# Kernel optimization log

Hardware: AMD Instinct MI355X
Metric: run time of the kernel (lower is better)

The kernel has to match this reference:

```python
import jax, jax.numpy as jnp
import numpy as np

B, S, E = 2, 2048, 2048
H, KVH = 16, 4
HD = E // H          # 128
REP = H // KVH       # 4
THETA = 100000.0


def _rope_cos_sin(seqlen, head_dim, theta=THETA):
    # Faithful to precompute_pos_cis: exponent is arange(0, d, 2) (NOT divided by d)
    freqs = 1.0 / theta ** jnp.arange(0, head_dim, 2, dtype=jnp.float32)[: head_dim // 2]
    ang = jnp.outer(jnp.arange(seqlen, dtype=jnp.float32), freqs)  # (S, HD/2)
    return jnp.cos(ang), jnp.sin(ang)


def _apply_rotary(t, cos, sin):
    # t: (B, S, h, HD) -> complex pairs along last dim
    b, s, h, d = t.shape
    t = t.astype(jnp.float32).reshape(b, s, h, d // 2, 2)
    tr, ti = t[..., 0], t[..., 1]
    c = cos[None, :, None, :]
    sn = sin[None, :, None, :]
    out_r = tr * c - ti * sn
    out_i = tr * sn + ti * c
    return jnp.stack([out_r, out_i], axis=-1).reshape(b, s, h, d)


def setup_inputs() -> dict:
    key = jax.random.key(0)
    ks = jax.random.split(key, 9)
    sc_e = 1.0 / np.sqrt(E)
    return {
        "x": jax.random.normal(ks[0], (B, S, E), jnp.float32),
        "wq": jax.random.normal(ks[1], (E, H * HD), jnp.float32) * sc_e,
        "bq": jax.random.normal(ks[2], (H * HD,), jnp.float32) * 0.01,
        "wk": jax.random.normal(ks[3], (E, KVH * HD), jnp.float32) * sc_e,
        "bk": jax.random.normal(ks[4], (KVH * HD,), jnp.float32) * 0.01,
        "wv": jax.random.normal(ks[5], (E, KVH * HD), jnp.float32) * sc_e,
        "bv": jax.random.normal(ks[6], (KVH * HD,), jnp.float32) * 0.01,
        "wo": jax.random.normal(ks[7], (H * HD, E), jnp.float32) * sc_e,
        "bo": jax.random.normal(ks[8], (E,), jnp.float32) * 0.01,
    }


def reference(x, wq, bq, wk, bk, wv, bv, wo, bo):
    b, s, _ = x.shape
    xq = (x @ wq + bq).reshape(b, s, H, HD)
    xk = (x @ wk + bk).reshape(b, s, KVH, HD)
    xv = (x @ wv + bv).reshape(b, s, KVH, HD)

    cos, sin = _rope_cos_sin(s, HD)
    xq = _apply_rotary(xq, cos, sin)
    xk = _apply_rotary(xk, cos, sin)

    # GQA: group query heads over shared KV heads instead of materializing repeat_kv
    q = xq.transpose(0, 2, 1, 3).reshape(b, KVH, REP, s, HD)  # (B, G, R, S, D)
    k = xk.transpose(0, 2, 1, 3)                               # (B, G, S, D)
    v = xv.astype(jnp.float32).transpose(0, 2, 1, 3)           # (B, G, S, D)

    scores = jnp.einsum("bgrqd,bgkd->bgrqk", q, k) / jnp.sqrt(jnp.float32(HD))
    causal = jnp.tril(jnp.ones((s, s), dtype=bool))
    scores = jnp.where(causal[None, None, None], scores, jnp.float32(-jnp.inf))
    attn = jax.nn.softmax(scores, axis=-1)
    out = jnp.einsum("bgrqk,bgkd->bgrqd", attn, v)  # (B, G, R, S, D)
    out = out.reshape(b, H, s, HD).transpose(0, 2, 1, 3).reshape(b, s, H * HD)
    return out @ wo + bo
```

## Files before the change

### kernel.cpp

```cpp
#include <hip/hip_runtime.h>
#include <math.h>

#define BB 2
#define SS 2048
#define EE 2048
#define HH 16
#define KVH 4
#define HD 128

typedef __attribute__((ext_vector_type(8))) short short8;
typedef __attribute__((ext_vector_type(4))) float f32x4;

__device__ __forceinline__ short f2b(float f) {
  unsigned u = __float_as_uint(f);
  unsigned r = (u + 0x7fffu + ((u >> 16) & 1u)) >> 16;
  return (short)r;
}

__device__ __forceinline__ void async_load16(const void* g, void* l) {
  __builtin_amdgcn_global_load_lds(
      (const __attribute__((address_space(1))) void*)g,
      (__attribute__((address_space(3))) void*)l, 16, 0, 0);
}

__device__ __forceinline__ float rope_freq(int jp) {
  return exp2f(-(float)(2 * jp) * 16.609640474436812f);
}

__global__ void f32_to_bf16(const float* __restrict__ in, short* __restrict__ out) {
  int i = (blockIdx.x * 256 + threadIdx.x) * 8;
  float4 a = *(const float4*)(in + i);
  float4 b = *(const float4*)(in + i + 4);
  short8 c;
  c[0] = f2b(a.x); c[1] = f2b(a.y); c[2] = f2b(a.z); c[3] = f2b(a.w);
  c[4] = f2b(b.x); c[5] = f2b(b.y); c[6] = f2b(b.z); c[7] = f2b(b.w);
  *(short8*)(out + i) = c;
}

__global__ void transpose_f2b(const float* __restrict__ in, short* __restrict__ out,
                              int K, int N) {
  __shared__ short tile[32][33];
  int n0 = blockIdx.x * 32, k0 = blockIdx.y * 32;
  int tx = threadIdx.x, ty = threadIdx.y;
#pragma unroll
  for (int i = 0; i < 32; i += 8)
    tile[ty + i][tx] = f2b(in[(size_t)(k0 + ty + i) * N + n0 + tx]);
  __syncthreads();
#pragma unroll
  for (int i = 0; i < 32; i += 8)
    out[(size_t)(n0 + ty + i) * K + k0 + tx] = tile[tx][ty + i];
}

__global__ __launch_bounds__(512, 4) void gemm_qkv(
    const short* __restrict__ A, const short* __restrict__ Bt,
    const float* __restrict__ bq, const float* __restrict__ bk,
    const float* __restrict__ bv,
    short* __restrict__ qbuf, short* __restrict__ kbuf, short* __restrict__ vtr) {
  __shared__ __align__(16) short Sm[256 * 136];
  short* Bl = Sm + 16384;
  const int K = EE;
  int t = threadIdx.x, lane = t & 63, w = t >> 6;
  int lj = lane & 15, lr = lane >> 4;
  int wm = (w >> 1) * 64, wn = (w & 1) * 64;
  int m0 = blockIdx.x * 256, n0 = blockIdx.y * 128;
  const short* Ab = A + (size_t)m0 * K;
  const short* Bb = Bt + (size_t)n0 * K;
  int srow = t >> 3, scol = (t & 7) * 8;
  char* ldsA = (char*)Sm + w * 1024;
  char* ldsB = (char*)Sm + 32768 + w * 1024;
  f32x4 acc[4][4] = {};
  for (int k0 = 0; k0 < K; k0 += 64) {
#pragma unroll
    for (int q = 0; q < 4; q++)
      async_load16(Ab + (size_t)(q * 64 + srow) * K + k0 + scol, ldsA + q * 8192);
#pragma unroll
    for (int q = 0; q < 2; q++)
      async_load16(Bb + (size_t)(q * 64 + srow) * K + k0 + scol, ldsB + q * 8192);
    __syncthreads();
    short8 a0[4], a1[4], b0[4], b1[4];
#pragma unroll
    for (int i = 0; i < 4; i++) {
      a0[i] = *(const short8*)&Sm[(wm + i * 16 + lj) * 64 + lr * 8];
      a1[i] = *(const short8*)&Sm[(wm + i * 16 + lj) * 64 + 32 + lr * 8];
    }
#pragma unroll
    for (int j = 0; j < 4; j++) {
      b0[j] = *(const short8*)&Bl[(wn + j * 16 + lj) * 64 + lr * 8];
      b1[j] = *(const short8*)&Bl[(wn + j * 16 + lj) * 64 + 32 + lr * 8];
    }
#pragma unroll
    for (int i = 0; i < 4; i++)
#pragma unroll
      for (int j = 0; j < 4; j++) {
        acc[i][j] = __builtin_amdgcn_mfma_f32_16x16x32_bf16(a0[i], b0[j], acc[i][j], 0, 0, 0);
        acc[i][j] = __builtin_amdgcn_mfma_f32_16x16x32_bf16(a1[i], b1[j], acc[i][j], 0, 0, 0);
      }
    __syncthreads();
  }
  if (n0 < 2048) {
#pragma unroll
    for (int j = 0; j < 4; j++) {
      int d = wn + j * 16 + lj;
      float bias = bq[n0 + d];
      float freq = rope_freq(d >> 1);
      bool odd = (d & 1) != 0;
#pragma unroll
      for (int i = 0; i < 4; i++)
#pragma unroll
        for (int r = 0; r < 4; r++) {
          int mloc = wm + i * 16 + lr * 4 + r;
          int s = (m0 + mloc) & (SS - 1);
          float val = acc[i][j][r] + bias;
          float other = __shfl_xor(val, 1, 64);
          float ang = (float)s * freq;
          float cs = cosf(ang), sn = sinf(ang);
          float res = odd ? (other * sn + val * cs) : (val * cs - other * sn);
          Sm[mloc * 136 + d] = f2b(res);
        }
    }
  } else if (n0 < 2560) {
    int base = n0 - 2048;
#pragma unroll
    for (int j = 0; j < 4; j++) {
      int d = wn + j * 16 + lj;
      float bias = bk[base + d];
      float freq = rope_freq(d >> 1);
      bool odd = (d & 1) != 0;
#pragma unroll
      for (int i = 0; i < 4; i++)
#pragma unroll
        for (int r = 0; r < 4; r++) {
          int mloc = wm + i * 16 + lr * 4 + r;
          int s = (m0 + mloc) & (SS - 1);
          float val = acc[i][j][r] + bias;
          float other = __shfl_xor(val, 1, 64);
          float ang = (float)s * freq;
          float cs = cosf(ang), sn = sinf(ang);
          float res = odd ? (other * sn + val * cs) : (val * cs - other * sn);
          Sm[mloc * 136 + d] = f2b(res);
        }
    }
  } else {
    int base = n0 - 2560;
#pragma unroll
    for (int j = 0; j < 4; j++) {
      int d = wn + j * 16 + lj;
      float bias = bv[base + d];
#pragma unroll
      for (int i = 0; i < 4; i++)
#pragma unroll
        for (int r = 0; r < 4; r++) {
          int mloc = wm + i * 16 + lr * 4 + r;
          Sm[d * 264 + mloc] = f2b(acc[i][j][r] + bias);
        }
    }
  }
  __syncthreads();
  if (n0 < 2048) {
    int r0 = t >> 4, ch = t & 15;
#pragma unroll
    for (int p = 0; p < 8; p++) {
      int row = p * 32 + r0;
      *(short8*)(qbuf + (size_t)(m0 + row) * 2048 + n0 + ch * 8) =
          *(const short8*)&Sm[row * 136 + ch * 8];
    }
  } else if (n0 < 2560) {
    int r0 = t >> 4, ch = t & 15;
    int kvh = (n0 - 2048) >> 7;
    int b = m0 >> 11, s0 = m0 & (SS - 1);
    short* dst = kbuf + ((size_t)(b * KVH + kvh) * SS + s0) * HD;
#pragma unroll
    for (int p = 0; p < 8; p++) {
      int row = p * 32 + r0;
      *(short8*)(dst + (size_t)row * HD + ch * 8) = *(const short8*)&Sm[row * 136 + ch * 8];
    }
  } else {
    int r0 = t >> 5, ch = t & 31;
    int kvh = (n0 - 2560) >> 7;
    int b = m0 >> 11, s0 = m0 & (SS - 1);
    short* dst = vtr + ((size_t)(b * KVH + kvh) * HD) * SS + s0;
#pragma unroll
    for (int p = 0; p < 8; p++) {
      int dl = p * 16 + r0;
      *(short8*)(dst + (size_t)dl * SS + ch * 8) = *(const short8*)&Sm[dl * 264 + ch * 8];
    }
  }
}

__global__ __launch_bounds__(256) void attn_kernel(
    const short* __restrict__ qb, const short* __restrict__ kb,
    const short* __restrict__ vt, short* __restrict__ ao) {
  __shared__ __align__(16) short Kl[64 * 128];
  __shared__ __align__(16) short Vl[128 * 64];
  __shared__ __align__(16) short Pl[4 * 16 * 64];
  int t = threadIdx.x, lane = t & 63, w = t >> 6;
  int lj = lane & 15, lr = lane >> 4;
  int id = blockIdx.x + (blockIdx.y << 5) + (blockIdx.z << 9);
  int swz = (id & 7) * 128 + (id >> 3);
  int qt = swz & 31, h = (swz >> 5) & 15, b = swz >> 9;
  int kvh = h >> 2;
  int qb0 = qt * 64;
  const short* qbase = qb + (size_t)(b * SS) * 2048 + h * HD;
  const short* kbase = kb + (size_t)(b * KVH + kvh) * SS * HD;
  const short* vbase = vt + (size_t)(b * KVH + kvh) * HD * SS;
  short8 aq[4];
  int sq = qb0 + w * 16 + lj;
#pragma unroll
  for (int kk = 0; kk < 4; kk++)
    aq[kk] = *(const short8*)(qbase + (size_t)sq * 2048 + kk * 32 + lr * 8);
  f32x4 O[8] = {};
  const float NEG = -1e30f;
  float mrow[4] = {NEG, NEG, NEG, NEG};
  float lrow[4] = {0.f, 0.f, 0.f, 0.f};
  const float scale = 0.088388347648318447f;
  int nkt = qt + 1;
  for (int kt = 0; kt < nkt; ++kt) {
    short8 gk[4], gv[4];
#pragma unroll
    for (int i = 0; i < 4; i++) {
      gk[i] = *(const short8*)(kbase + (size_t)(kt * 64 + i * 16 + (t >> 4)) * HD + (t & 15) * 8);
      gv[i] = *(const short8*)(vbase + (size_t)(i * 32 + (t >> 3)) * SS + kt * 64 + (t & 7) * 8);
    }
#pragma unroll
    for (int i = 0; i < 4; i++) {
      *(short8*)&Kl[(i * 16 + (t >> 4)) * 128 + (t & 15) * 8] = gk[i];
      *(short8*)&Vl[(i * 32 + (t >> 3)) * 64 + (t & 7) * 8] = gv[i];
    }
    __syncthreads();
    f32x4 S[4];
#pragma unroll
    for (int nt = 0; nt < 4; nt++) {
      f32x4 sc = {};
#pragma unroll
      for (int kk = 0; kk < 4; kk++) {
        short8 bk_ = *(const short8*)&Kl[(nt * 16 + lj) * 128 + kk * 32 + lr * 8];
        sc = __builtin_amdgcn_mfma_f32_16x16x32_bf16(aq[kk], bk_, sc, 0, 0, 0);
      }
      S[nt] = sc;
    }
    int rowg = qb0 + w * 16 + lr * 4;
#pragma unroll
    for (int nt = 0; nt < 4; nt++) {
      int colg = kt * 64 + nt * 16 + lj;
#pragma unroll
      for (int r = 0; r < 4; r++) {
        float v = S[nt][r] * scale;
        if (colg > rowg + r) v = NEG;
        S[nt][r] = v;
      }
    }
    float alpha[4];
#pragma unroll
    for (int r = 0; r < 4; r++) {
      float m_ = fmaxf(fmaxf(S[0][r], S[1][r]), fmaxf(S[2][r], S[3][r]));
#pragma unroll
      for (int off = 1; off < 16; off <<= 1) m_ = fmaxf(m_, __shfl_xor(m_, off, 64));
      float mn = fmaxf(mrow[r], m_);
      alpha[r] = __expf(mrow[r] - mn);
      mrow[r] = mn;
    }
    float ls[4] = {0.f, 0.f, 0.f, 0.f};
#pragma unroll
    for (int nt = 0; nt < 4; nt++)
#pragma unroll
      for (int r = 0; r < 4; r++) {
        float p = __expf(S[nt][r] - mrow[r]);
        ls[r] += p;
        Pl[(w * 16 + lr * 4 + r) * 64 + nt * 16 + lj] = f2b(p);
      }
#pragma unroll
    for (int r = 0; r < 4; r++) {
      float s_ = ls[r];
#pragma unroll
      for (int off = 1; off < 16; off <<= 1) s_ += __shfl_xor(s_, off, 64);
      lrow[r] = lrow[r] * alpha[r] + s_;
    }
#pragma unroll
    for (int jt = 0; jt < 8; jt++)
#pragma unroll
      for (int r = 0; r < 4; r++) O[jt][r] *= alpha[r];
#pragma unroll
    for (int kk = 0; kk < 2; kk++) {
      short8 ap = *(const short8*)&Pl[(w * 16 + lj) * 64 + kk * 32 + lr * 8];
#pragma unroll
      for (int jt = 0; jt < 8; jt++) {
        short8 bv_ = *(const short8*)&Vl[(jt * 16 + lj) * 64 + kk * 32 + lr * 8];
        O[jt] = __builtin_amdgcn_mfma_f32_16x16x32_bf16(ap, bv_, O[jt], 0, 0, 0);
      }
    }
    __syncthreads();
  }
  size_t obase = (size_t)(b * SS + qb0 + w * 16) * 2048 + h * HD;
#pragma unroll
  for (int jt = 0; jt < 8; jt++)
#pragma unroll
    for (int r = 0; r < 4; r++) {
      int row = lr * 4 + r;
      ao[obase + (size_t)row * 2048 + jt * 16 + lj] = f2b(O[jt][r] / lrow[r]);
    }
}

__global__ __launch_bounds__(512, 4) void gemm_out(
    const short* __restrict__ A, const short* __restrict__ Bt,
    const float* __restrict__ bo, float* __restrict__ out) {
  __shared__ __align__(16) short Sm[24576];
  short* Bl = Sm + 16384;
  const int K = EE;
  int t = threadIdx.x, lane = t & 63, w = t >> 6;
  int lj = lane & 15, lr = lane >> 4;
  int wm = (w >> 1) * 64, wn = (w & 1) * 64;
  int m0 = blockIdx.x * 256, n0 = blockIdx.y * 128;
  const short* Ab = A + (size_t)m0 * K;
  const short* Bb = Bt + (size_t)n0 * K;
  int srow = t >> 3, scol = (t & 7) * 8;
  char* ldsA = (char*)Sm + w * 1024;
  char* ldsB = (char*)Sm + 32768 + w * 1024;
  f32x4 acc[4][4] = {};
  for (int k0 = 0; k0 < K; k0 += 64) {
#pragma unroll
    for (int q = 0; q < 4; q++)
      async_load16(Ab + (size_t)(q * 64 + srow) * K + k0 + scol, ldsA + q * 8192);
#pragma unroll
    for (int q = 0; q < 2; q++)
      async_load16(Bb + (size_t)(q * 64 + srow) * K + k0 + scol, ldsB + q * 8192);
    __syncthreads();
    short8 a0[4], a1[4], b0[4], b1[4];
#pragma unroll
    for (int i = 0; i < 4; i++) {
      a0[i] = *(const short8*)&Sm[(wm + i * 16 + lj) * 64 + lr * 8];
      a1[i] = *(const short8*)&Sm[(wm + i * 16 + lj) * 64 + 32 + lr * 8];
    }
#pragma unroll
    for (int j = 0; j < 4; j++) {
      b0[j] = *(const short8*)&Bl[(wn + j * 16 + lj) * 64 + lr * 8];
      b1[j] = *(const short8*)&Bl[(wn + j * 16 + lj) * 64 + 32 + lr * 8];
    }
#pragma unroll
    for (int i = 0; i < 4; i++)
#pragma unroll
      for (int j = 0; j < 4; j++) {
        acc[i][j] = __builtin_amdgcn_mfma_f32_16x16x32_bf16(a0[i], b0[j], acc[i][j], 0, 0, 0);
        acc[i][j] = __builtin_amdgcn_mfma_f32_16x16x32_bf16(a1[i], b1[j], acc[i][j], 0, 0, 0);
      }
    __syncthreads();
  }
#pragma unroll
  for (int j = 0; j < 4; j++) {
    int n = n0 + wn + j * 16 + lj;
    float bias = bo[n];
#pragma unroll
    for (int i = 0; i < 4; i++)
#pragma unroll
      for (int r = 0; r < 4; r++) {
        int m = m0 + wm + i * 16 + lr * 4 + r;
        out[(size_t)m * 2048 + n] = acc[i][j][r] + bias;
      }
  }
}

extern "C" void kernel_launch(void* const* d_in, const int* in_sizes, int n_in,
                              void* d_out, int out_size, void* d_ws, size_t ws_size,
                              hipStream_t stream) {
  const float* x  = (const float*)d_in[0];
  const float* wq = (const float*)d_in[1];
  const float* bq = (const float*)d_in[2];
  const float* wk = (const float*)d_in[3];
  const float* bk = (const float*)d_in[4];
  const float* wv = (const float*)d_in[5];
  const float* bv = (const float*)d_in[6];
  const float* wo = (const float*)d_in[7];
  const float* bo = (const float*)d_in[8];
  float* out = (float*)d_out;

  short* W1t = (short*)d_ws;
  short* Wot = W1t + (size_t)3072 * 2048;
  short* qb_ = Wot + (size_t)2048 * 2048;
  short* kb_ = qb_ + (size_t)4096 * 2048;
  short* vt_ = kb_ + (size_t)4096 * 512;
  short* ao_ = vt_ + (size_t)4096 * 512;
  short* xb_ = ao_;

  dim3 tb(32, 8);
  f32_to_bf16<<<4096, 256, 0, stream>>>(x, xb_);
  transpose_f2b<<<dim3(64, 64), tb, 0, stream>>>(wq, W1t, 2048, 2048);
  transpose_f2b<<<dim3(16, 64), tb, 0, stream>>>(wk, W1t + (size_t)2048 * 2048, 2048, 512);
  transpose_f2b<<<dim3(16, 64), tb, 0, stream>>>(wv, W1t + (size_t)2560 * 2048, 2048, 512);
  transpose_f2b<<<dim3(64, 64), tb, 0, stream>>>(wo, Wot, 2048, 2048);

  gemm_qkv<<<dim3(16, 24), 512, 0, stream>>>(xb_, W1t, bq, bk, bv, qb_, kb_, vt_);
  attn_kernel<<<dim3(32, 16, 2), 256, 0, stream>>>(qb_, kb_, vt_, ao_);
  gemm_out<<<dim3(16, 16), 512, 0, stream>>>(ao_, Wot, bo, out);
}
```

Baseline: 982.8 us.

## Shrink QKV GEMM tile to 128x128 and prefetch next K/V tile in attention

The QKV projection GEMM now runs 256-thread blocks on 128x128 tiles instead of 512 threads on 256x128, which doubles the grid and halves LDS per block, with the epilogue strides adjusted to match. The attention kernel loads the next K/V tile into registers while the current tile is in use, with a manual waitcnt and barrier, so global-load latency is hidden behind the matrix math. It also raises wave priority around the MFMA sections. The costs are higher register pressure from the prefetch buffers and less data reuse per block in the GEMM.

```diff
diff --git a/kernel.cpp b/kernel.cpp
--- a/kernel.cpp
+++ b/kernel.cpp
@@ -51,37 +51,37 @@
     out[(size_t)(n0 + ty + i) * K + k0 + tx] = tile[tx][ty + i];
 }
 
-__global__ __launch_bounds__(512, 4) void gemm_qkv(
+__global__ __launch_bounds__(256) void gemm_qkv(
     const short* __restrict__ A, const short* __restrict__ Bt,
     const float* __restrict__ bq, const float* __restrict__ bk,
     const float* __restrict__ bv,
     short* __restrict__ qbuf, short* __restrict__ kbuf, short* __restrict__ vtr) {
-  __shared__ __align__(16) short Sm[256 * 136];
-  short* Bl = Sm + 16384;
+  __shared__ __align__(16) short Sm[128 * 136];
+  short* Al = Sm;
+  short* Bl = Sm + 128 * 64;
   const int K = EE;
   int t = threadIdx.x, lane = t & 63, w = t >> 6;
-  int lj = lane & 15, lr = lane >> 4;
   int wm = (w >> 1) * 64, wn = (w & 1) * 64;
-  int m0 = blockIdx.x * 256, n0 = blockIdx.y * 128;
+  int m0 = blockIdx.x * 128, n0 = blockIdx.y * 128;
   const short* Ab = A + (size_t)m0 * K;
   const short* Bb = Bt + (size_t)n0 * K;
   int srow = t >> 3, scol = (t & 7) * 8;
-  char* ldsA = (char*)Sm + w * 1024;
-  char* ldsB = (char*)Sm + 32768 + w * 1024;
+  int lj = lane & 15, lr = lane >> 4;
   f32x4 acc[4][4] = {};
   for (int k0 = 0; k0 < K; k0 += 64) {
 #pragma unroll
-    for (int q = 0; q < 4; q++)
-      async_load16(Ab + (size_t)(q * 64 + srow) * K + k0 + scol, ldsA + q * 8192);
-#pragma unroll
-    for (int q = 0; q < 2; q++)
-      async_load16(Bb + (size_t)(q * 64 + srow) * K + k0 + scol, ldsB + q * 8192);
+    for (int q = 0; q < 4; q++) {
+      async_load16(Ab + (size_t)(q * 32 + srow) * K + k0 + scol,
+                   (char*)Al + q * 4096 + w * 1024);
+      async_load16(Bb + (size_t)(q * 32 + srow) * K + k0 + scol,
+                   (char*)Bl + q * 4096 + w * 1024);
+    }
     __syncthreads();
     short8 a0[4], a1[4], b0[4], b1[4];
 #pragma unroll
     for (int i = 0; i < 4; i++) {
-      a0[i] = *(const short8*)&Sm[(wm + i * 16 + lj) * 64 + lr * 8];
-      a1[i] = *(const short8*)&Sm[(wm + i * 16 + lj) * 64 + 32 + lr * 8];
+      a0[i] = *(const short8*)&Al[(wm + i * 16 + lj) * 64 + lr * 8];
+      a1[i] = *(const short8*)&Al[(wm + i * 16 + lj) * 64 + 32 + lr * 8];
     }
 #pragma unroll
     for (int j = 0; j < 4; j++) {
@@ -151,38 +151,36 @@
 #pragma unroll
         for (int r = 0; r < 4; r++) {
           int mloc = wm + i * 16 + lr * 4 + r;
-          Sm[d * 264 + mloc] = f2b(acc[i][j][r] + bias);
+          Sm[d * 136 + mloc] = f2b(acc[i][j][r] + bias);
         }
     }
   }
   __syncthreads();
+  int r0 = t >> 4, ch = t & 15;
   if (n0 < 2048) {
-    int r0 = t >> 4, ch = t & 15;
 #pragma unroll
     for (int p = 0; p < 8; p++) {
-      int row = p * 32 + r0;
+      int row = p * 16 + r0;
       *(short8*)(qbuf + (size_t)(m0 + row) * 2048 + n0 + ch * 8) =
           *(const short8*)&Sm[row * 136 + ch * 8];
     }
   } else if (n0 < 2560) {
-    int r0 = t >> 4, ch = t & 15;
     int kvh = (n0 - 2048) >> 7;
     int b = m0 >> 11, s0 = m0 & (SS - 1);
     short* dst = kbuf + ((size_t)(b * KVH + kvh) * SS + s0) * HD;
 #pragma unroll
     for (int p = 0; p < 8; p++) {
-      int row = p * 32 + r0;
+      int row = p * 16 + r0;
       *(short8*)(dst + (size_t)row * HD + ch * 8) = *(const short8*)&Sm[row * 136 + ch * 8];
     }
   } else {
-    int r0 = t >> 5, ch = t & 31;
     int kvh = (n0 - 2560) >> 7;
     int b = m0 >> 11, s0 = m0 & (SS - 1);
     short* dst = vtr + ((size_t)(b * KVH + kvh) * HD) * SS + s0;
 #pragma unroll
     for (int p = 0; p < 8; p++) {
-      int dl = p * 16 + r0;
-      *(short8*)(dst + (size_t)dl * SS + ch * 8) = *(const short8*)&Sm[dl * 264 + ch * 8];
+      int row = p * 16 + r0;
+      *(short8*)(dst + (size_t)row * SS + ch * 8) = *(const short8*)&Sm[row * 136 + ch * 8];
     }
   }
 }
@@ -214,20 +212,31 @@
   float lrow[4] = {0.f, 0.f, 0.f, 0.f};
   const float scale = 0.088388347648318447f;
   int nkt = qt + 1;
+  short8 gk[4], gv[4];
+#pragma unroll
+  for (int i = 0; i < 4; i++) {
+    gk[i] = *(const short8*)(kbase + (size_t)(i * 16 + (t >> 4)) * HD + (t & 15) * 8);
+    gv[i] = *(const short8*)(vbase + (size_t)(i * 32 + (t >> 3)) * SS + (t & 7) * 8);
+  }
   for (int kt = 0; kt < nkt; ++kt) {
-    short8 gk[4], gv[4];
-#pragma unroll
-    for (int i = 0; i < 4; i++) {
-      gk[i] = *(const short8*)(kbase + (size_t)(kt * 64 + i * 16 + (t >> 4)) * HD + (t & 15) * 8);
-      gv[i] = *(const short8*)(vbase + (size_t)(i * 32 + (t >> 3)) * SS + kt * 64 + (t & 7) * 8);
-    }
 #pragma unroll
     for (int i = 0; i < 4; i++) {
       *(short8*)&Kl[(i * 16 + (t >> 4)) * 128 + (t & 15) * 8] = gk[i];
       *(short8*)&Vl[(i * 32 + (t >> 3)) * 64 + (t & 7) * 8] = gv[i];
     }
-    __syncthreads();
+    if (kt + 1 < nkt) {
+#pragma unroll
+      for (int i = 0; i < 4; i++) {
+        gk[i] = *(const short8*)(kbase +
+                 (size_t)((kt + 1) * 64 + i * 16 + (t >> 4)) * HD + (t & 15) * 8);
+        gv[i] = *(const short8*)(vbase +
+                 (size_t)(i * 32 + (t >> 3)) * SS + (kt + 1) * 64 + (t & 7) * 8);
+      }
+    }
+    asm volatile("s_waitcnt lgkmcnt(0)" ::: "memory");
+    __builtin_amdgcn_s_barrier();
     f32x4 S[4];
+    __builtin_amdgcn_s_setprio(1);
 #pragma unroll
     for (int nt = 0; nt < 4; nt++) {
       f32x4 sc = {};
@@ -238,6 +247,7 @@
       }
       S[nt] = sc;
     }
+    __builtin_amdgcn_s_setprio(0);
     int rowg = qb0 + w * 16 + lr * 4;
 #pragma unroll
     for (int nt = 0; nt < 4; nt++) {
@@ -279,6 +289,7 @@
     for (int jt = 0; jt < 8; jt++)
 #pragma unroll
       for (int r = 0; r < 4; r++) O[jt][r] *= alpha[r];
+    __builtin_amdgcn_s_setprio(1);
 #pragma unroll
     for (int kk = 0; kk < 2; kk++) {
       short8 ap = *(const short8*)&Pl[(w * 16 + lj) * 64 + kk * 32 + lr * 8];
@@ -288,6 +299,7 @@
         O[jt] = __builtin_amdgcn_mfma_f32_16x16x32_bf16(ap, bv_, O[jt], 0, 0, 0);
       }
     }
+    __builtin_amdgcn_s_setprio(0);
     __syncthreads();
   }
   size_t obase = (size_t)(b * SS + qb0 + w * 16) * 2048 + h * HD;
@@ -387,7 +399,7 @@
   transpose_f2b<<<dim3(16, 64), tb, 0, stream>>>(wv, W1t + (size_t)2560 * 2048, 2048, 512);
   transpose_f2b<<<dim3(64, 64), tb, 0, stream>>>(wo, Wot, 2048, 2048);
 
-  gemm_qkv<<<dim3(16, 24), 512, 0, stream>>>(xb_, W1t, bq, bk, bv, qb_, kb_, vt_);
+  gemm_qkv<<<dim3(32, 24), 256, 0, stream>>>(xb_, W1t, bq, bk, bv, qb_, kb_, vt_);
   attn_kernel<<<dim3(32, 16, 2), 256, 0, stream>>>(qb_, kb_, vt_, ao_);
   gemm_out<<<dim3(16, 16), 512, 0, stream>>>(ao_, Wot, bo, out);
 }
```

Measured after the change: 914.0 us. 1.08x faster.
